# Kernel optimization log

Hardware: AMD Instinct MI355X
Metric: run time of the kernel (lower is better)

## Reference

```python
import jax, jax.numpy as jnp
import numpy as np

B, N, M, C, KV, H = 2, 1024, 2048, 1024, 768, 16
D = C // H
SCALE = D ** -0.5  # qk_scale defaults to head_dim**-0.5


def setup_inputs() -> dict:
    key = jax.random.key(0)
    ks = jax.random.split(key, 8)
    return {
        "q": jax.random.normal(ks[0], (B, N, C), jnp.float32),
        "kv": jax.random.normal(ks[1], (B, M, KV), jnp.float32),
        "alibi_bias": jax.random.normal(ks[2], (B, H, N, M), jnp.float32) * 0.02,
        "padding_mask": jax.random.randint(ks[3], (B, M), 0, 2).astype(bool),
        "Wq": jax.random.normal(ks[4], (C, C), jnp.float32) * 0.02,
        "Wkv": jax.random.normal(ks[5], (2 * C, KV), jnp.float32) * 0.02,
        "Wproj": jax.random.normal(ks[6], (C, C), jnp.float32) * 0.02,
        "bproj": jnp.zeros((C,), jnp.float32),
    }


def reference(q, kv, alibi_bias, Wq, Wkv, Wproj, bproj, padding_mask):
    Bq, Nq, Cq = q.shape
    # q projection -> (B, H, N, D)
    qh = (q @ Wq.T).reshape(Bq, Nq, H, D).transpose(0, 2, 1, 3)
    # kv projection -> (2, B, H, M, D)
    kvp = (kv @ Wkv.T).reshape(Bq, -1, 2, H, D).transpose(2, 0, 3, 1, 4)
    k, v = kvp[0], kvp[1]
    # scaled dot-product scores (B, H, N, M)
    attn = jnp.einsum('bhnd,bhmd->bhnm', qh * SCALE, k)
    attn = attn + alibi_bias
    attn = jnp.where(padding_mask[:, None, None, :], -jnp.inf, attn)
    # softmax in fp32, cast back to q dtype (matches torch softmax(dtype=float32))
    attn = jax.nn.softmax(attn.astype(jnp.float32), axis=-1).astype(q.dtype)
    x = jnp.einsum('bhnm,bhmd->bhnd', attn, v).transpose(0, 2, 1, 3).reshape(Bq, Nq, Cq)
    return x @ Wproj.T + bproj
```

## Files before the change

kernel.cpp:

```cpp
#include <hip/hip_runtime.h>
#include <hip/hip_bf16.h>
#include <hip/hip_fp16.h>

#define B_  2
#define N_  1024
#define M_  2048
#define C_  1024
#define KV_ 768
#define H_  16
#define D_  64

typedef _Float16 half8 __attribute__((ext_vector_type(8)));
typedef float f32x4 __attribute__((ext_vector_type(4)));

__device__ inline void gload16(const _Float16* g, _Float16* l) {
    __builtin_amdgcn_global_load_lds(
        (const __attribute__((address_space(1))) unsigned int*)g,
        (__attribute__((address_space(3))) unsigned int*)l, 16, 0, 0);
}

#define NQ4  (B_ * N_ * C_ / 4)
#define NKV4 (B_ * M_ * KV_ / 4)
#define NWQ4 (C_ * C_ / 4)
#define NWK4 (2 * C_ * KV_ / 4)
#define NTOT4 (NQ4 + NKV4 + NWQ4 + NWK4 + NWQ4)

__global__ __launch_bounds__(256)
void cvt_all(const float* __restrict__ q, const float* __restrict__ kv,
             const float* __restrict__ Wq, const float* __restrict__ Wkv,
             const float* __restrict__ Wp,
             _Float16* __restrict__ qh, _Float16* __restrict__ kvh,
             _Float16* __restrict__ Wqh, _Float16* __restrict__ Wkvh,
             _Float16* __restrict__ Wph)
{
    int i = blockIdx.x * 256 + threadIdx.x;
    if (i >= NTOT4) return;
    const float* s; _Float16* d; int off; float sc = 1.0f;
    if (i < NQ4)                          { s = q;   d = qh;   off = i; sc = 0.125f; }
    else if (i < NQ4 + NKV4)              { s = kv;  d = kvh;  off = i - NQ4; }
    else if (i < NQ4 + NKV4 + NWQ4)       { s = Wq;  d = Wqh;  off = i - NQ4 - NKV4; }
    else if (i < NQ4 + NKV4 + NWQ4 + NWK4){ s = Wkv; d = Wkvh; off = i - NQ4 - NKV4 - NWQ4; }
    else                                  { s = Wp;  d = Wph;  off = i - NQ4 - NKV4 - NWQ4 - NWK4; }
    float4 v = ((const float4*)s)[off];
    union { _Float16 h[4]; unsigned long long u; } pk;
    pk.h[0] = (_Float16)(v.x * sc); pk.h[1] = (_Float16)(v.y * sc);
    pk.h[2] = (_Float16)(v.z * sc); pk.h[3] = (_Float16)(v.w * sc);
    ((unsigned long long*)d)[off] = pk.u;
}

template<int ND, int KD, int EPI>
__device__ __forceinline__
void gemm_body(const _Float16* A, const _Float16* Bm, void* out0, void* out1,
               _Float16* As, _Float16* Bs, int bx, int by)
{
    const int tid  = threadIdx.x;
    const int lane = tid & 63;
    const int w    = tid >> 6;
    const int l16  = lane & 15;
    const int quad = lane >> 4;
    const int wm   = w >> 1, wn = w & 1;
    const int m0   = by * 128;
    const int n0   = bx * 128;

    const int srow = tid >> 2;
    const int scol = ((tid & 3) ^ (srow & 3)) * 8;
    const int ldso = srow * 32 + (tid & 3) * 8;

    f32x4 acc[4][4];
    {
        f32x4 z = {0.f, 0.f, 0.f, 0.f};
        for (int i = 0; i < 4; i++) for (int j = 0; j < 4; j++) acc[i][j] = z;
    }

    for (int k0 = 0; k0 < KD; k0 += 32) {
        __syncthreads();
        gload16(A  + (size_t)(m0 + srow)      * KD + k0 + scol, As + ldso);
        gload16(A  + (size_t)(m0 + 64 + srow) * KD + k0 + scol, As + 64 * 32 + ldso);
        gload16(Bm + (size_t)(n0 + srow)      * KD + k0 + scol, Bs + ldso);
        gload16(Bm + (size_t)(n0 + 64 + srow) * KD + k0 + scol, Bs + 64 * 32 + ldso);
        __syncthreads();

        half8 af[4], bf[4];
        #pragma unroll
        for (int i = 0; i < 4; i++) {
            int r = wm * 64 + i * 16 + l16;
            af[i] = *(const half8*)&As[r * 32 + ((quad ^ (r & 3)) * 8)];
        }
        #pragma unroll
        for (int j = 0; j < 4; j++) {
            int r = wn * 64 + j * 16 + l16;
            bf[j] = *(const half8*)&Bs[r * 32 + ((quad ^ (r & 3)) * 8)];
        }
        #pragma unroll
        for (int i = 0; i < 4; i++)
            #pragma unroll
            for (int j = 0; j < 4; j++)
                acc[i][j] = __builtin_amdgcn_mfma_f32_16x16x32_f16(af[i], bf[j], acc[i][j], 0, 0, 0);
    }

    #pragma unroll
    for (int i = 0; i < 4; i++)
        #pragma unroll
        for (int j = 0; j < 4; j++) {
            int mb = m0 + wm * 64 + i * 16 + quad * 4;
            int n  = n0 + wn * 64 + j * 16 + l16;
            if (EPI == 0) {
                #pragma unroll
                for (int r = 0; r < 4; r++)
                    ((_Float16*)out0)[(size_t)(mb + r) * ND + n] = (_Float16)acc[i][j][r];
            } else {
                int b = mb >> 11, ml = mb & 2047;
                if (n < C_) {
                    int h = n >> 6, d = n & 63;
                    #pragma unroll
                    for (int r = 0; r < 4; r++)
                        ((_Float16*)out0)[((size_t)(b * H_ + h) * M_ + ml + r) * D_ + d] =
                            (_Float16)acc[i][j][r];
                } else {
                    int h = (n >> 6) & 15, d = n & 63;
                    union { _Float16 h4[4]; unsigned long long u; } pk;
                    #pragma unroll
                    for (int r = 0; r < 4; r++) pk.h4[r] = (_Float16)acc[i][j][r];
                    *(unsigned long long*)&((_Float16*)out1)[((size_t)(b * H_ + h) * D_ + d) * M_ + ml] = pk.u;
                }
            }
        }
}

__global__ __launch_bounds__(256)
void qkv_gemm(const _Float16* __restrict__ qh, const _Float16* __restrict__ Wqh,
              _Float16* __restrict__ qp,
              const _Float16* __restrict__ kvh, const _Float16* __restrict__ Wkvh,
              _Float16* __restrict__ k_ws, _Float16* __restrict__ v_ws)
{
    __shared__ _Float16 As[128 * 32];
    __shared__ _Float16 Bs[128 * 32];
    int id = blockIdx.x;
    if (id < 128)
        gemm_body<C_, C_, 0>(qh, Wqh, qp, nullptr, As, Bs, id & 7, id >> 3);
    else {
        int r = id - 128;
        gemm_body<2 * C_, KV_, 1>(kvh, Wkvh, k_ws, v_ws, As, Bs, r & 15, r >> 4);
    }
}

__global__ __launch_bounds__(256)
void outproj(const _Float16* __restrict__ A, const _Float16* __restrict__ Bm,
             float* __restrict__ out, const float* __restrict__ bias)
{
    __shared__ _Float16 As[64 * 32];
    __shared__ _Float16 Bs[64 * 32];

    const int tid  = threadIdx.x;
    const int lane = tid & 63;
    const int w    = tid >> 6;
    const int l16  = lane & 15;
    const int quad = lane >> 4;
    const int wm   = w >> 1, wn = w & 1;
    const int m0   = blockIdx.y * 64;
    const int n0   = blockIdx.x * 64;

    const int srow = tid >> 2;
    const int scol = ((tid & 3) ^ (srow & 3)) * 8;
    const int ldso = srow * 32 + (tid & 3) * 8;

    f32x4 acc[2][2];
    {
        f32x4 z = {0.f, 0.f, 0.f, 0.f};
        for (int i = 0; i < 2; i++) for (int j = 0; j < 2; j++) acc[i][j] = z;
    }

    for (int k0 = 0; k0 < C_; k0 += 32) {
        __syncthreads();
        gload16(A  + (size_t)(m0 + srow) * C_ + k0 + scol, As + ldso);
        gload16(Bm + (size_t)(n0 + srow) * C_ + k0 + scol, Bs + ldso);
        __syncthreads();

        half8 af[2], bf[2];
        #pragma unroll
        for (int i = 0; i < 2; i++) {
            int r = wm * 32 + i * 16 + l16;
            af[i] = *(const half8*)&As[r * 32 + ((quad ^ (r & 3)) * 8)];
        }
        #pragma unroll
        for (int j = 0; j < 2; j++) {
            int r = wn * 32 + j * 16 + l16;
            bf[j] = *(const half8*)&Bs[r * 32 + ((quad ^ (r & 3)) * 8)];
        }
        #pragma unroll
        for (int i = 0; i < 2; i++)
            #pragma unroll
            for (int j = 0; j < 2; j++)
                acc[i][j] = __builtin_amdgcn_mfma_f32_16x16x32_f16(af[i], bf[j], acc[i][j], 0, 0, 0);
    }

    #pragma unroll
    for (int i = 0; i < 2; i++)
        #pragma unroll
        for (int j = 0; j < 2; j++)
            #pragma unroll
            for (int r = 0; r < 4; r++) {
                int m = m0 + wm * 32 + i * 16 + quad * 4 + r;
                int n = n0 + wn * 32 + j * 16 + l16;
                out[(size_t)m * C_ + n] = acc[i][j][r] + bias[n];
            }
}

__global__ __launch_bounds__(256, 2)
void flash_attn(const _Float16* __restrict__ qw, const _Float16* __restrict__ kw,
                const _Float16* __restrict__ vw, const float* __restrict__ alibi,
                const void* __restrict__ pmask, _Float16* __restrict__ xw)
{
    __shared__ _Float16 Ps[4][16][136];

    const int tid  = threadIdx.x;
    const int lane = tid & 63;
    const int w    = tid >> 6;
    const int l16  = lane & 15;
    const int quad = lane >> 4;

    const int bid = blockIdx.x;
    const int wk  = (bid & 7) * 64 + (bid >> 3);
    const int bh  = wk >> 4;
    const int b   = bh >> 4;
    const int h   = bh & 15;
    const int n0  = (wk & 15) * 64;

    unsigned am = ((const unsigned*)pmask)[lane] & 0xFFFFFF00u;
    const int mi = (__ballot(am != 0) == 0ull) ? 1 : 0;

    half8 qf[2];
    {
        const _Float16* qp = qw + ((size_t)(b * N_ + n0 + w * 16 + l16) * C_) + h * 64 + quad * 8;
        qf[0] = *(const half8*)qp;
        qf[1] = *(const half8*)(qp + 32);
    }

    f32x4 accO[4];
    float rs[4];
    {
        f32x4 z = {0.f, 0.f, 0.f, 0.f};
        for (int i = 0; i < 4; i++) accO[i] = z;
    }
    #pragma unroll
    for (int r = 0; r < 4; r++) rs[r] = 0.f;

    const _Float16* kbase = kw + (size_t)bh * (M_ * D_);
    const _Float16* vbase = vw + (size_t)bh * (D_ * M_);
    const float*    abase = alibi + (size_t)bh * ((size_t)N_ * M_) + (size_t)n0 * M_
                          + (size_t)(w * 16 + quad * 4) * M_;
    const unsigned char* pm8  = (const unsigned char*)pmask;
    const int*           pm32 = (const int*)pmask;

    float alA[8][4], alB[8][4];
    int   mkA[8],    mkB[8];

    auto prefetch = [&](float (&al)[8][4], int (&mk)[8], int m0) {
        #pragma unroll
        for (int j = 0; j < 8; j++) {
            int mcol = m0 + j * 16 + l16;
            mk[j] = mi ? pm32[b * M_ + mcol] : (int)pm8[b * M_ + mcol];
            const float* ap = abase + mcol;
            #pragma unroll
            for (int r = 0; r < 4; r++) al[j][r] = ap[(size_t)r * M_];
        }
    };

    auto chunk = [&](int m0, float (&al)[8][4], int (&mk)[8],
                     float (&alN)[8][4], int (&mkN)[8], bool pref) {
        half8 kf[8][2];
        #pragma unroll
        for (int j = 0; j < 8; j++) {
            const _Float16* kp = kbase + (size_t)(m0 + j * 16 + l16) * D_ + quad * 8;
            kf[j][0] = *(const half8*)kp;
            kf[j][1] = *(const half8*)(kp + 32);
        }
        f32x4 s[8];
        {
            f32x4 z = {0.f, 0.f, 0.f, 0.f};
            #pragma unroll
            for (int j = 0; j < 8; j++) s[j] = z;
        }
        #pragma unroll
        for (int j = 0; j < 8; j++) {
            s[j] = __builtin_amdgcn_mfma_f32_16x16x32_f16(qf[0], kf[j][0], s[j], 0, 0, 0);
            s[j] = __builtin_amdgcn_mfma_f32_16x16x32_f16(qf[1], kf[j][1], s[j], 0, 0, 0);
        }

        half8 vf[4][4];
        #pragma unroll
        for (int kk = 0; kk < 4; kk++)
            #pragma unroll
            for (int dt = 0; dt < 4; dt++)
                vf[kk][dt] = *(const half8*)(vbase + (size_t)(dt * 16 + l16) * M_
                                             + m0 + kk * 32 + quad * 8);

        if (pref) prefetch(alN, mkN, m0 + 128);

        #pragma unroll
        for (int j = 0; j < 8; j++)
            #pragma unroll
            for (int r = 0; r < 4; r++) {
                float sv = fminf(s[j][r] + al[j][r], 11.0f);
                float p  = exp2f(sv * 1.44269504f);
                p = mk[j] ? 0.f : p;
                rs[r] += p;
                Ps[w][quad * 4 + r][j * 16 + l16] = (_Float16)p;
            }

        #pragma unroll
        for (int kk = 0; kk < 4; kk++) {
            half8 pf = *(const half8*)&Ps[w][l16][kk * 32 + quad * 8];
            #pragma unroll
            for (int dt = 0; dt < 4; dt++)
                accO[dt] = __builtin_amdgcn_mfma_f32_16x16x32_f16(pf, vf[kk][dt], accO[dt], 0, 0, 0);
        }
    };

    prefetch(alA, mkA, 0);
    for (int m0 = 0; m0 < M_; m0 += 256) {
        chunk(m0,       alA, mkA, alB, mkB, true);
        chunk(m0 + 128, alB, mkB, alA, mkA, m0 + 256 < M_);
    }

    #pragma unroll
    for (int off = 1; off < 16; off <<= 1)
        #pragma unroll
        for (int r = 0; r < 4; r++) rs[r] += __shfl_xor(rs[r], off, 64);
    float inv[4];
    #pragma unroll
    for (int r = 0; r < 4; r++) inv[r] = 1.0f / rs[r];

    #pragma unroll
    for (int dt = 0; dt < 4; dt++)
        #pragma unroll
        for (int r = 0; r < 4; r++) {
            int n = n0 + w * 16 + quad * 4 + r;
            xw[(size_t)(b * N_ + n) * C_ + h * 64 + dt * 16 + l16] =
                (_Float16)(accO[dt][r] * inv[r]);
        }
}

extern "C" void kernel_launch(void* const* d_in, const int* in_sizes, int n_in,
                              void* d_out, int out_size, void* d_ws, size_t ws_size,
                              hipStream_t stream)
{
    const float* q     = (const float*)d_in[0];
    const float* kv    = (const float*)d_in[1];
    const float* alibi = (const float*)d_in[2];
    const void*  pmask = d_in[3];
    const float* Wq    = (const float*)d_in[4];
    const float* Wkv   = (const float*)d_in[5];
    const float* Wproj = (const float*)d_in[6];
    const float* bproj = (const float*)d_in[7];
    float* out = (float*)d_out;

    const size_t MB = 1u << 20;
    char* ws = (char*)d_ws;
    _Float16* qh     = (_Float16*)(ws + 0 * MB);
    _Float16* kvh    = (_Float16*)(ws + 4 * MB);
    _Float16* Wqh    = (_Float16*)(ws + 12 * MB);
    _Float16* Wkvh   = (_Float16*)(ws + 14 * MB);
    _Float16* Wprojh = (_Float16*)(ws + 18 * MB);
    _Float16* qp     = (_Float16*)(ws + 20 * MB);
    _Float16* k_ws   = (_Float16*)(ws + 24 * MB);
    _Float16* v_ws   = (_Float16*)(ws + 33 * MB);
    _Float16* x_ws   = (_Float16*)(ws + 42 * MB);

    cvt_all<<<(NTOT4 + 255) / 256, 256, 0, stream>>>(
        q, kv, Wq, Wkv, Wproj, qh, kvh, Wqh, Wkvh, Wprojh);

    qkv_gemm<<<640, 256, 0, stream>>>(qh, Wqh, qp, kvh, Wkvh, k_ws, v_ws);

    flash_attn<<<512, 256, 0, stream>>>(
        qp, k_ws, v_ws, alibi, pmask, x_ws);

    outproj<<<dim3(C_ / 64, (B_ * N_) / 64), 256, 0, stream>>>(
        x_ws, Wprojh, out, bproj);
}
```

Baseline: 518.2 us.

## Stage alibi tiles into swizzled LDS via async global-to-LDS loads

The attention kernel used to prefetch the alibi bias into per-lane registers with scalar 4-byte strided loads, double-buffered across 128-column chunks. It now copies 64-column alibi tiles into a double-buffered, XOR-swizzled LDS buffer with 16-byte global_load_lds transfers, issued after the softmax step so they overlap the PV MFMAs. The chunk width drops to 64 columns, which lowers register pressure and shrinks the P staging buffer. In exchange it uses an extra 32KB of LDS per block. It also relies on the compiler inserting correct waits for the asynchronous LDS writes, since there is no explicit wait or barrier before Al is read.

```diff
diff --git a/kernel.cpp b/kernel.cpp
--- a/kernel.cpp
+++ b/kernel.cpp
@@ -14,6 +14,11 @@
 typedef float f32x4 __attribute__((ext_vector_type(4)));
 
 __device__ inline void gload16(const _Float16* g, _Float16* l) {
+    __builtin_amdgcn_global_load_lds(
+        (const __attribute__((address_space(1))) unsigned int*)g,
+        (__attribute__((address_space(3))) unsigned int*)l, 16, 0, 0);
+}
+__device__ inline void gload16f(const float* g, float* l) {
     __builtin_amdgcn_global_load_lds(
         (const __attribute__((address_space(1))) unsigned int*)g,
         (__attribute__((address_space(3))) unsigned int*)l, 16, 0, 0);
@@ -211,7 +216,8 @@
                 const _Float16* __restrict__ vw, const float* __restrict__ alibi,
                 const void* __restrict__ pmask, _Float16* __restrict__ xw)
 {
-    __shared__ _Float16 Ps[4][16][136];
+    __shared__ _Float16 Ps[4][16][72];
+    __shared__ __align__(16) float Al[2][64][64];
 
     const int tid  = threadIdx.x;
     const int lane = tid & 63;
@@ -247,80 +253,85 @@
 
     const _Float16* kbase = kw + (size_t)bh * (M_ * D_);
     const _Float16* vbase = vw + (size_t)bh * (D_ * M_);
-    const float*    abase = alibi + (size_t)bh * ((size_t)N_ * M_) + (size_t)n0 * M_
-                          + (size_t)(w * 16 + quad * 4) * M_;
+    const float*    arow  = alibi + (size_t)bh * ((size_t)N_ * M_) + (size_t)n0 * M_;
     const unsigned char* pm8  = (const unsigned char*)pmask;
     const int*           pm32 = (const int*)pmask;
 
-    float alA[8][4], alB[8][4];
-    int   mkA[8],    mkB[8];
-
-    auto prefetch = [&](float (&al)[8][4], int (&mk)[8], int m0) {
-        #pragma unroll
-        for (int j = 0; j < 8; j++) {
-            int mcol = m0 + j * 16 + l16;
-            mk[j] = mi ? pm32[b * M_ + mcol] : (int)pm8[b * M_ + mcol];
-            const float* ap = abase + mcol;
-            #pragma unroll
-            for (int r = 0; r < 4; r++) al[j][r] = ap[(size_t)r * M_];
+    auto stage = [&](int st) {
+        #pragma unroll
+        for (int c = 0; c < 4; c++) {
+            int rbase = w * 16 + c * 4;
+            int rr    = rbase + (lane >> 4);
+            int uu    = (lane & 15) ^ (2 * ((w * 4 + c) & 3));
+            const float* src = arow + (size_t)rr * M_ + st * 64 + uu * 4;
+            gload16f(src, &Al[st & 1][rbase][0]);
         }
     };
 
-    auto chunk = [&](int m0, float (&al)[8][4], int (&mk)[8],
-                     float (&alN)[8][4], int (&mkN)[8], bool pref) {
-        half8 kf[8][2];
-        #pragma unroll
-        for (int j = 0; j < 8; j++) {
+    stage(0);
+
+    for (int st = 0; st < M_ / 64; st++) {
+        const int m0 = st * 64;
+
+        half8 kf[4][2];
+        #pragma unroll
+        for (int j = 0; j < 4; j++) {
             const _Float16* kp = kbase + (size_t)(m0 + j * 16 + l16) * D_ + quad * 8;
             kf[j][0] = *(const half8*)kp;
             kf[j][1] = *(const half8*)(kp + 32);
         }
-        f32x4 s[8];
-        {
-            f32x4 z = {0.f, 0.f, 0.f, 0.f};
-            #pragma unroll
-            for (int j = 0; j < 8; j++) s[j] = z;
-        }
-        #pragma unroll
-        for (int j = 0; j < 8; j++) {
-            s[j] = __builtin_amdgcn_mfma_f32_16x16x32_f16(qf[0], kf[j][0], s[j], 0, 0, 0);
-            s[j] = __builtin_amdgcn_mfma_f32_16x16x32_f16(qf[1], kf[j][1], s[j], 0, 0, 0);
-        }
-
-        half8 vf[4][4];
-        #pragma unroll
-        for (int kk = 0; kk < 4; kk++)
+        half8 vf[2][4];
+        #pragma unroll
+        for (int kk = 0; kk < 2; kk++)
             #pragma unroll
             for (int dt = 0; dt < 4; dt++)
                 vf[kk][dt] = *(const half8*)(vbase + (size_t)(dt * 16 + l16) * M_
                                              + m0 + kk * 32 + quad * 8);
-
-        if (pref) prefetch(alN, mkN, m0 + 128);
-
-        #pragma unroll
-        for (int j = 0; j < 8; j++)
+        int mk[4];
+        #pragma unroll
+        for (int j = 0; j < 4; j++) {
+            int mcol = m0 + j * 16 + l16;
+            mk[j] = mi ? pm32[b * M_ + mcol] : (int)pm8[b * M_ + mcol];
+        }
+
+        f32x4 s[4];
+        {
+            f32x4 z = {0.f, 0.f, 0.f, 0.f};
+            #pragma unroll
+            for (int j = 0; j < 4; j++) s[j] = z;
+        }
+        #pragma unroll
+        for (int j = 0; j < 4; j++) {
+            s[j] = __builtin_amdgcn_mfma_f32_16x16x32_f16(qf[0], kf[j][0], s[j], 0, 0, 0);
+            s[j] = __builtin_amdgcn_mfma_f32_16x16x32_f16(qf[1], kf[j][1], s[j], 0, 0, 0);
+        }
+
+        #pragma unroll
+        for (int j = 0; j < 4; j++) {
+            int pu = (j * 4 + (l16 >> 2)) ^ (2 * quad);
+            int pc = pu * 4 + (l16 & 3);
             #pragma unroll
             for (int r = 0; r < 4; r++) {
-                float sv = fminf(s[j][r] + al[j][r], 11.0f);
+                float alv = Al[st & 1][w * 16 + quad * 4 + r][pc];
+                float sv = fminf(s[j][r] + alv, 11.0f);
                 float p  = exp2f(sv * 1.44269504f);
                 p = mk[j] ? 0.f : p;
                 rs[r] += p;
                 Ps[w][quad * 4 + r][j * 16 + l16] = (_Float16)p;
             }
-
-        #pragma unroll
-        for (int kk = 0; kk < 4; kk++) {
+        }
+
+        __builtin_amdgcn_sched_barrier(0);
+        if (st + 1 < M_ / 64) stage(st + 1);
+        __builtin_amdgcn_sched_barrier(0);
+
+        #pragma unroll
+        for (int kk = 0; kk < 2; kk++) {
             half8 pf = *(const half8*)&Ps[w][l16][kk * 32 + quad * 8];
             #pragma unroll
             for (int dt = 0; dt < 4; dt++)
                 accO[dt] = __builtin_amdgcn_mfma_f32_16x16x32_f16(pf, vf[kk][dt], accO[dt], 0, 0, 0);
         }
-    };
-
-    prefetch(alA, mkA, 0);
-    for (int m0 = 0; m0 < M_; m0 += 256) {
-        chunk(m0,       alA, mkA, alB, mkB, true);
-        chunk(m0 + 128, alB, mkB, alA, mkA, m0 + 256 < M_);
     }
 
     #pragma unroll
```

New measurement: 504.3 us. 1.03x faster.
